# Kernel tuning notes

Hardware: AMD Instinct MI355X
Metric: run time of the kernel (lower is better)

## Reference

```python
import jax, jax.numpy as jnp
import numpy as np

NUM_HEADS = 16
EPS_LN = 1e-5
EPS_NORM = 1e-12


def layernorm(x, g, b):
    mu = jnp.mean(x, axis=-1, keepdims=True)
    var = jnp.mean((x - mu) ** 2, axis=-1, keepdims=True)
    return (x - mu) * jax.lax.rsqrt(var + EPS_LN) * g + b


def l2norm(x):
    n = jnp.sqrt(jnp.sum(x * x, axis=-1, keepdims=True))
    return x / jnp.maximum(n, EPS_NORM)


def setup_inputs() -> dict:
    key = jax.random.key(0)
    ks = jax.random.split(key, 12)
    B, N, C = 8, 1024, 1024
    std = 0.02
    inp = {
        "txt_token": jax.random.normal(ks[0], (B, 1, C), jnp.float32),
        "text_features": jax.random.normal(ks[1], (B, N, C), jnp.float32),
        "text_mask": jax.random.randint(ks[2], (B, N), 0, 2).astype(bool),
        "vis_token": jax.random.normal(ks[3], (B, 1, C), jnp.float32),
        "top_lens": 256,
        # parameters
        "Wqkv": jax.random.normal(ks[4], (C, 3 * C), jnp.float32) * std,
        "bqkv": jnp.zeros((3 * C,), jnp.float32),
        "Wp2": jax.random.normal(ks[5], (C, C), jnp.float32) * std,
        "bp2": jnp.zeros((C,), jnp.float32),
        "ln2_g": jnp.ones((C,), jnp.float32),
        "ln2_b": jnp.zeros((C,), jnp.float32),
        "sim_alpha": jnp.ones((1,), jnp.float32),
        "sim_beta": jnp.zeros((1,), jnp.float32),
        "Wp1": jax.random.normal(ks[6], (C, C), jnp.float32) * std,
        "bp1": jnp.zeros((C,), jnp.float32),
        "ln1_g": jnp.ones((C,), jnp.float32),
        "ln1_b": jnp.zeros((C,), jnp.float32),
    }
    return inp


def reference(txt_token, text_features, text_mask, vis_token, top_lens,
              Wqkv, bqkv, Wp2, bp2, ln2_g, ln2_b,
              sim_alpha, sim_beta, Wp1, bp1, ln1_g, ln1_b):
    B, N, C = text_features.shape
    H = NUM_HEADS
    hd = C // H
    scale = hd ** (-0.5)

    qkv = (text_features @ Wqkv + bqkv).reshape(B, N, 3, H, hd)
    q = qkv[:, :, 0].transpose(0, 2, 1, 3)  # [B,H,N,hd]
    k = qkv[:, :, 1].transpose(0, 2, 1, 3)
    v = qkv[:, :, 2].transpose(0, 2, 1, 3)

    attn = jnp.einsum('bhqd,bhkd->bhqk', q, k) * scale  # [B,H,N,N]
    vals, idx = jax.lax.top_k(attn, top_lens)            # [B,H,N,k]
    p = jax.nn.softmax(vals, axis=-1)

    # scatter topk softmax back into zeros at original key positions
    b_ix = jnp.arange(B)[:, None, None, None]
    h_ix = jnp.arange(H)[None, :, None, None]
    q_ix = jnp.arange(N)[None, None, :, None]
    attn_sp = jnp.zeros_like(attn).at[b_ix, h_ix, q_ix, idx].set(p)

    # mask padded keys, then second softmax (dropout = identity in eval)
    attn_sp = jnp.where(text_mask[:, None, None, :], -jnp.inf, attn_sp)
    attn_w = jax.nn.softmax(attn_sp, axis=-1)

    x = jnp.einsum('bhqk,bhkd->bqhd', attn_w, v).reshape(B, N, C)
    x = x @ Wp2 + bp2
    tf = layernorm(text_features + x, ln2_g, ln2_b)  # [B,N,C]

    # cosine-similarity top-k pooling
    sim = sim_beta + sim_alpha * jnp.einsum('bmc,bnc->bmn', l2norm(vis_token), l2norm(tf))  # [B,1,N]
    sim = jax.nn.sigmoid(jnp.where(text_mask[:, None, :], -jnp.inf, sim))
    _, top_idx = jax.lax.top_k(sim, top_lens)        # [B,1,k]
    top_idx = top_idx[:, 0]                           # [B,k]
    top_vecs = jnp.take_along_axis(tf, top_idx[:, :, None], axis=1)  # [B,k,C]
    pooled = jnp.mean(top_vecs, axis=1, keepdims=True)               # [B,1,C]

    tt = pooled + txt_token
    tt = layernorm(tt @ Wp1 + bp1, ln1_g, ln1_b)
    return tt, tf
```

## Files before the change

### kernel.cpp

```cpp
#include <hip/hip_runtime.h>
#include <stdint.h>

typedef unsigned short u16;
typedef float floatx4 __attribute__((ext_vector_type(4)));
typedef short short8 __attribute__((ext_vector_type(8)));

#define TOPK_ 256

#define AS1(p) ((const __attribute__((address_space(1))) void*)(p))
#define AS3(p) ((__attribute__((address_space(3))) void*)(p))

__device__ __forceinline__ u16 f2bf(float f) {
  unsigned u = __builtin_bit_cast(unsigned, f);
  unsigned r = (u + 0x7FFFu + ((u >> 16) & 1u)) >> 16;
  return (u16)r;
}
__device__ __forceinline__ float bf2f(u16 b) {
  unsigned u = ((unsigned)b) << 16;
  return __builtin_bit_cast(float, u);
}

__device__ __forceinline__ float wave_sum_f32(float x) {
#define DPP_STEP(ctrl, rmask)                                                        \
  {                                                                                  \
    float t_ = __builtin_bit_cast(                                                   \
        float, __builtin_amdgcn_update_dpp(0, __builtin_bit_cast(int, x), ctrl,      \
                                           rmask, 0xf, true));                       \
    x += t_;                                                                         \
  }
  DPP_STEP(0x111, 0xf)
  DPP_STEP(0x112, 0xf)
  DPP_STEP(0x114, 0xf)
  DPP_STEP(0x118, 0xf)
  DPP_STEP(0x142, 0xa)
  DPP_STEP(0x143, 0xc)
#undef DPP_STEP
  return __builtin_bit_cast(float,
                            __builtin_amdgcn_readlane(__builtin_bit_cast(int, x), 63));
}

__device__ __forceinline__ void wave_sum2_f32(float& x, float& y) {
#define DPP_STEP2(ctrl, rmask)                                                       \
  {                                                                                  \
    float tx_ = __builtin_bit_cast(                                                  \
        float, __builtin_amdgcn_update_dpp(0, __builtin_bit_cast(int, x), ctrl,      \
                                           rmask, 0xf, true));                       \
    float ty_ = __builtin_bit_cast(                                                  \
        float, __builtin_amdgcn_update_dpp(0, __builtin_bit_cast(int, y), ctrl,      \
                                           rmask, 0xf, true));                       \
    x += tx_;                                                                        \
    y += ty_;                                                                        \
  }
  DPP_STEP2(0x111, 0xf)
  DPP_STEP2(0x112, 0xf)
  DPP_STEP2(0x114, 0xf)
  DPP_STEP2(0x118, 0xf)
  DPP_STEP2(0x142, 0xa)
  DPP_STEP2(0x143, 0xc)
#undef DPP_STEP2
  x = __builtin_bit_cast(float, __builtin_amdgcn_readlane(__builtin_bit_cast(int, x), 63));
  y = __builtin_bit_cast(float, __builtin_amdgcn_readlane(__builtin_bit_cast(int, y), 63));
}

__device__ __forceinline__ float block_sum256(float v, volatile float* scratch, int wave,
                                              int lane) {
#pragma unroll
  for (int o = 32; o > 0; o >>= 1) v += __shfl_xor(v, o);
  __syncthreads();
  if (lane == 0) scratch[wave] = v;
  __syncthreads();
  return scratch[0] + scratch[1] + scratch[2] + scratch[3];
}

__global__ __launch_bounds__(256) void prep_kernel(const float* __restrict__ text,
                                                   u16* __restrict__ Abf,
                                                   const float* __restrict__ Wqkv,
                                                   u16* __restrict__ Wtqkv,
                                                   const float* __restrict__ Wp2,
                                                   u16* __restrict__ Wtp2,
                                                   const float* __restrict__ vis,
                                                   float* __restrict__ vhat) {
  __shared__ u16 tile[32][33];
  __shared__ float red[4];
  int blk = blockIdx.x, t = threadIdx.x;
  if (blk < 8192) {
    int i = (blk * 256 + t) * 4;
    float4 v = *reinterpret_cast<const float4*>(text + i);
    ushort4 o;
    o.x = f2bf(v.x); o.y = f2bf(v.y); o.z = f2bf(v.z); o.w = f2bf(v.w);
    *reinterpret_cast<ushort4*>(Abf + i) = o;
  } else if (blk < 12288) {
    const float* W;
    u16* Wt;
    int cols, id;
    if (blk < 11264) { W = Wqkv; Wt = Wtqkv; cols = 3072; id = blk - 8192; }
    else             { W = Wp2;  Wt = Wtp2;  cols = 1024; id = blk - 11264; }
    int nx = cols >> 5;
    int n0 = (id % nx) * 32, k0 = (id / nx) * 32;
    int r = t >> 3, c4 = (t & 7) * 4;
    float4 v = *reinterpret_cast<const float4*>(W + (size_t)(k0 + r) * cols + n0 + c4);
    tile[r][c4 + 0] = f2bf(v.x);
    tile[r][c4 + 1] = f2bf(v.y);
    tile[r][c4 + 2] = f2bf(v.z);
    tile[r][c4 + 3] = f2bf(v.w);
    __syncthreads();
    ushort4 o;
    o.x = tile[c4 + 0][r]; o.y = tile[c4 + 1][r];
    o.z = tile[c4 + 2][r]; o.w = tile[c4 + 3][r];
    *reinterpret_cast<ushort4*>(Wt + (size_t)(n0 + r) * 1024 + k0 + c4) = o;
  } else {
    int b = blk - 12288, wave = t >> 6, lane = t & 63;
    float4 vv = *reinterpret_cast<const float4*>(vis + b * 1024 + t * 4);
    float sq = vv.x * vv.x + vv.y * vv.y + vv.z * vv.z + vv.w * vv.w;
    sq = block_sum256(sq, red, wave, lane);
    float inv = 1.f / fmaxf(sqrtf(sq), 1e-12f);
    float4 o = make_float4(vv.x * inv, vv.y * inv, vv.z * inv, vv.w * inv);
    *reinterpret_cast<float4*>(vhat + b * 1024 + t * 4) = o;
  }
}

__global__ __launch_bounds__(256) void gemm_bt(const u16* __restrict__ A,
                                               const u16* __restrict__ Bt,
                                               const float* __restrict__ bias,
                                               int M, int Nn, int K, int mode,
                                               u16* __restrict__ qb, u16* __restrict__ kb,
                                               u16* __restrict__ vb, u16* __restrict__ yb) {
  __shared__ __align__(16) u16 SMEM[9216];
  u16* As = SMEM;
  u16* Bs = SMEM + 4096;
  int id = blockIdx.x + blockIdx.y * gridDim.x;
  int cpx = (gridDim.x * gridDim.y) >> 3;
  int swz = (id & 7) * cpx + (id >> 3);
  int bx = swz % gridDim.x, by = swz / gridDim.x;
  int m0 = by * 128, n0 = bx * 128;
  int t = threadIdx.x, lane = t & 63, wave = t >> 6;
  int wr = wave >> 1, wc = wave & 1;
  int lrow = lane & 15, lko = (lane >> 4) * 8;
  floatx4 acc[4][4];
#pragma unroll
  for (int i = 0; i < 4; ++i)
#pragma unroll
    for (int j = 0; j < 4; ++j) acc[i][j] = (floatx4){0.f, 0.f, 0.f, 0.f};
  int srow = t >> 2, sc8 = (t & 3) * 8;
  const u16* gA0 = A + (size_t)(m0 + srow) * K + sc8;
  const u16* gA1 = A + (size_t)(m0 + srow + 64) * K + sc8;
  const u16* gB0 = Bt + (size_t)(n0 + srow) * K + sc8;
  const u16* gB1 = Bt + (size_t)(n0 + srow + 64) * K + sc8;
  for (int k0 = 0; k0 < K; k0 += 32) {
    __syncthreads();
    __builtin_amdgcn_global_load_lds(AS1(gA0 + k0), AS3(&As[t * 8]), 16, 0, 0);
    __builtin_amdgcn_global_load_lds(AS1(gA1 + k0), AS3(&As[t * 8 + 2048]), 16, 0, 0);
    __builtin_amdgcn_global_load_lds(AS1(gB0 + k0), AS3(&Bs[t * 8]), 16, 0, 0);
    __builtin_amdgcn_global_load_lds(AS1(gB1 + k0), AS3(&Bs[t * 8 + 2048]), 16, 0, 0);
    __syncthreads();
    short8 afr[4], bfr[4];
#pragma unroll
    for (int i = 0; i < 4; ++i) {
      afr[i] = *reinterpret_cast<const short8*>(&As[(wr * 64 + i * 16 + lrow) * 32 + lko]);
      bfr[i] = *reinterpret_cast<const short8*>(&Bs[(wc * 64 + i * 16 + lrow) * 32 + lko]);
    }
#pragma unroll
    for (int i = 0; i < 4; ++i)
#pragma unroll
      for (int j = 0; j < 4; ++j)
        acc[i][j] = __builtin_amdgcn_mfma_f32_16x16x32_bf16(afr[i], bfr[j], acc[i][j], 0, 0, 0);
  }
  int rb = (lane >> 4) * 4;
  if (mode == 0 && n0 >= 2048) {
#pragma unroll
    for (int i = 0; i < 4; ++i) {
#pragma unroll
      for (int j = 0; j < 4; ++j) {
        int gcol = n0 + wc * 64 + j * 16 + lrow;
        float bv = bias[gcol];
        int grow0 = m0 + wr * 64 + i * 16 + rb;
        int cc = gcol & 1023, hh = cc >> 6, dd = cc & 63;
        int bb = grow0 >> 10, nq0 = grow0 & 1023;
        size_t headq = ((size_t)bb * 16 + hh);
        int dtile = dd >> 4, drow = dd & 15;
        int ks32 = nq0 >> 5, kk = nq0 & 31, lq = kk >> 3, e = kk & 7;
        int lane2 = lq * 16 + drow;
        ushort4 o;
        o.x = f2bf(acc[i][j][0] + bv);
        o.y = f2bf(acc[i][j][1] + bv);
        o.z = f2bf(acc[i][j][2] + bv);
        o.w = f2bf(acc[i][j][3] + bv);
        *reinterpret_cast<ushort4*>(vb + headq * 65536 + (size_t)ks32 * 2048 +
                                    dtile * 512 + lane2 * 8 + e) = o;
      }
    }
  } else {
    u16* LDSC = SMEM;
    for (int half = 0; half < 2; ++half) {
      __syncthreads();
      if (wc == half) {
#pragma unroll
        for (int i = 0; i < 4; ++i)
#pragma unroll
          for (int j = 0; j < 4; ++j) {
            float bv = bias[n0 + half * 64 + j * 16 + lrow];
#pragma unroll
            for (int rr = 0; rr < 4; ++rr)
              LDSC[(wr * 64 + i * 16 + rb + rr) * 72 + j * 16 + lrow] =
                  f2bf(acc[i][j][rr] + bv);
          }
      }
      __syncthreads();
      int row = t >> 4, c4 = (t & 15) * 4;
#pragma unroll
      for (int it = 0; it < 8; ++it) {
        int rw = row + it * 16;
        ushort4 val = *reinterpret_cast<const ushort4*>(&LDSC[rw * 72 + c4]);
        int grow = m0 + rw, gcol = n0 + half * 64 + c4;
        if (mode == 1) {
          *reinterpret_cast<ushort4*>(yb + (size_t)grow * 1024 + gcol) = val;
        } else {
          int sec = gcol >> 10, cc = gcol & 1023, hh = cc >> 6, dd = cc & 63;
          int bb = grow >> 10, nq = grow & 1023;
          size_t head = ((size_t)bb * 16 + hh);
          if (sec == 0) {
            *reinterpret_cast<ushort4*>(qb + (head * 1024 + nq) * 64 + dd) = val;
          } else {
            int kc = nq >> 4, krow = nq & 15;
            int p = dd >> 5, quad = (dd >> 3) & 3, e = dd & 7;
            *reinterpret_cast<ushort4*>(kb + head * 65536 + (size_t)kc * 1024 +
                                        p * 512 + (quad * 16 + krow) * 8 + e) = val;
          }
        }
      }
    }
  }
}

#define SSTR 1036
__global__ __launch_bounds__(512, 8) void attn_kernel(const u16* __restrict__ qb,
                                                      const u16* __restrict__ kb,
                                                      const u16* __restrict__ vb,
                                                      const int* __restrict__ mask,
                                                      u16* __restrict__ xout) {
  extern __shared__ __align__(16) char smem[];
  u16* Sb = reinterpret_cast<u16*>(smem);
  u16* qs = reinterpret_cast<u16*>(smem + 33152);
  unsigned char* mk8 = reinterpret_cast<unsigned char*>(smem + 35456);
  float* invZs = reinterpret_cast<float*>(smem + 36480);
  float* part = reinterpret_cast<float*>(smem + 36544);

  int blk = blockIdx.x;
  int bh = blk >> 6, qt = blk & 63;
  int b = bh >> 4, h = bh & 15;
  int t = threadIdx.x, wave = t >> 6, lane = t & 63;
  const u16* qh = qb + ((size_t)bh * 1024 + qt * 16) * 64;
  const u16* kh = kb + (size_t)bh * 65536;
  const u16* vh = vb + (size_t)bh * 65536;

  {
    int2 mm = *reinterpret_cast<const int2*>(mask + b * 1024 + t * 2);
    u16 pk = (u16)((mm.x != 0 ? 1u : 0u) | ((mm.y != 0 ? 1u : 0u) << 8));
    *reinterpret_cast<u16*>(&mk8[t * 2]) = pk;
  }
  if (t < 256) {
    int row = t >> 4, c4 = (t & 15) * 4;
    *reinterpret_cast<ushort4*>(&qs[row * 72 + c4]) =
        *reinterpret_cast<const ushort4*>(qh + row * 64 + c4);
  }
  __syncthreads();

  int lrow = lane & 15, lko = (lane >> 4) * 8;
  int quad = lane >> 4;
  int dtile = wave & 3, kq = wave >> 2;
  const u16* vbase = vh + (size_t)(kq * 16 * 4 + dtile) * 512 + lane * 8;

  {
    short8 qf0 = *reinterpret_cast<const short8*>(&qs[lrow * 72 + lko]);
    short8 qf1 = *reinterpret_cast<const short8*>(&qs[lrow * 72 + lko + 32]);
#pragma unroll 4
    for (int c = 0; c < 8; ++c) {
      int kc = wave * 8 + c;
      const u16* kt = kh + (size_t)kc * 1024 + lane * 8;
      short8 kf0 = *reinterpret_cast<const short8*>(kt);
      short8 kf1 = *reinterpret_cast<const short8*>(kt + 512);
      floatx4 acc = (floatx4){0.f, 0.f, 0.f, 0.f};
      acc = __builtin_amdgcn_mfma_f32_16x16x32_bf16(kf0, qf0, acc, 0, 0, 0);
      acc = __builtin_amdgcn_mfma_f32_16x16x32_bf16(kf1, qf1, acc, 0, 0, 0);
      unsigned kk[4];
#pragma unroll
      for (int i = 0; i < 4; ++i) {
        float f = __builtin_fmaf(acc[i], 64.f, 4096.f);
        f = __builtin_amdgcn_fmed3f(f, 0.f, 8191.f);
        kk[i] = (unsigned)f;
      }
      uint2 pk;
      pk.x = __builtin_amdgcn_perm(kk[1], kk[0], 0x05040100u);
      pk.y = __builtin_amdgcn_perm(kk[3], kk[2], 0x05040100u);
      *reinterpret_cast<uint2*>(&Sb[lrow * SSTR + kc * 16 + quad * 4]) = pk;
    }
  }
  __syncthreads();

  short8 vp0 = *reinterpret_cast<const short8*>(vbase);
  short8 vp1 = *reinterpret_cast<const short8*>(vbase + 2048);
  short8 vp2 = *reinterpret_cast<const short8*>(vbase + 4096);
  short8 vp3 = *reinterpret_cast<const short8*>(vbase + 6144);
  asm volatile("" : "+v"(vp0), "+v"(vp1), "+v"(vp2), "+v"(vp3));

  {
    const u16* SrA = Sb + (wave * 2) * SSTR;
    const u16* SrB = Sb + (wave * 2 + 1) * SSTR;
    unsigned kA[16], kB[16];
#pragma unroll
    for (int jj = 0; jj < 4; ++jj) {
      uint2 pa = *reinterpret_cast<const uint2*>(SrA + 4 * lane + 256 * jj);
      uint2 pb = *reinterpret_cast<const uint2*>(SrB + 4 * lane + 256 * jj);
      kA[4 * jj + 0] = pa.x & 0xffffu; kA[4 * jj + 1] = pa.x >> 16;
      kA[4 * jj + 2] = pa.y & 0xffffu; kA[4 * jj + 3] = pa.y >> 16;
      kB[4 * jj + 0] = pb.x & 0xffffu; kB[4 * jj + 1] = pb.x >> 16;
      kB[4 * jj + 2] = pb.y & 0xffffu; kB[4 * jj + 3] = pb.y >> 16;
    }
    unsigned TA = 0, TB = 0;
    int dA = 0, dB = 0;
    for (int bit = 12; bit >= 5; --bit) {
      unsigned cA = TA | (1u << bit), cB = TB | (1u << bit);
      int cntA = 0, cntB = 0;
#pragma unroll
      for (int i = 0; i < 16; ++i) {
        cntA += (int)__popcll(__ballot(kA[i] >= cA));
        cntB += (int)__popcll(__ballot(kB[i] >= cB));
      }
      if (!dA && cntA >= TOPK_) { TA = cA; if (cntA == TOPK_) dA = 1; }
      if (!dB && cntB >= TOPK_) { TB = cB; if (cntB == TOPK_) dB = 1; }
      if (dA && dB) break;
    }
    unsigned mm[4];
#pragma unroll
    for (int jj = 0; jj < 4; ++jj)
      mm[jj] = *reinterpret_cast<const unsigned*>(mk8 + 4 * lane + 256 * jj);
    const float C1 = 1.44269504f / 512.f;
    const float C0 = -4096.f * (1.44269504f / 512.f);
#pragma unroll 1
    for (int rr = 0; rr < 2; ++rr) {
      int row = wave * 2 + rr;
      unsigned T = rr ? TB : TA;
      unsigned kk[16];
      if (rr == 0) {
#pragma unroll
        for (int i = 0; i < 16; ++i) kk[i] = kA[i];
      } else {
        const u16* Sr = Sb + row * SSTR;
#pragma unroll
        for (int jj = 0; jj < 4; ++jj) {
          uint2 p = *reinterpret_cast<const uint2*>(Sr + 4 * lane + 256 * jj);
          kk[4 * jj + 0] = p.x & 0xffffu; kk[4 * jj + 1] = p.x >> 16;
          kk[4 * jj + 2] = p.y & 0xffffu; kk[4 * jj + 3] = p.y >> 16;
        }
      }
      float e[16];
      float seq[4] = {0.f, 0.f, 0.f, 0.f};
#pragma unroll
      for (int i = 0; i < 16; ++i) {
        float ex = __builtin_amdgcn_exp2f(__builtin_fmaf((float)kk[i], C1, C0));
        ex = (kk[i] >= T) ? ex : 0.f;
        e[i] = ex;
        seq[i & 3] += ex;
      }
      float se = wave_sum_f32((seq[0] + seq[1]) + (seq[2] + seq[3]));
      float cB2 = __builtin_amdgcn_rcpf(se) * 1.44269504f;
      float Z = 0.f;
      u16* Wr = Sb + row * SSTR;
#pragma unroll
      for (int jj = 0; jj < 4; ++jj) {
        unsigned m = mm[jj];
        float w0 = __builtin_amdgcn_exp2f(e[4 * jj + 0] * cB2);
        float w1 = __builtin_amdgcn_exp2f(e[4 * jj + 1] * cB2);
        float w2 = __builtin_amdgcn_exp2f(e[4 * jj + 2] * cB2);
        float w3 = __builtin_amdgcn_exp2f(e[4 * jj + 3] * cB2);
        w0 = (m & 0x000000ffu) ? 0.f : w0;
        w1 = (m & 0x0000ff00u) ? 0.f : w1;
        w2 = (m & 0x00ff0000u) ? 0.f : w2;
        w3 = (m & 0xff000000u) ? 0.f : w3;
        Z += (w0 + w1) + (w2 + w3);
        uint2 pw;
        pw.x = __builtin_amdgcn_perm(__builtin_bit_cast(unsigned, w1),
                                     __builtin_bit_cast(unsigned, w0), 0x07060302u);
        pw.y = __builtin_amdgcn_perm(__builtin_bit_cast(unsigned, w3),
                                     __builtin_bit_cast(unsigned, w2), 0x07060302u);
        *reinterpret_cast<uint2*>(Wr + 4 * lane + 256 * jj) = pw;
      }
      Z = wave_sum_f32(Z);
      if (lane == 0) invZs[row] = __builtin_amdgcn_rcpf(Z);
    }
  }
  __syncthreads();

  {
    floatx4 acc = (floatx4){0.f, 0.f, 0.f, 0.f};
    const u16* wrow = Sb + lrow * SSTR + kq * 512;
    short8 af;
    af = *reinterpret_cast<const short8*>(wrow + 0 * 32 + lko);
    acc = __builtin_amdgcn_mfma_f32_16x16x32_bf16(af, vp0, acc, 0, 0, 0);
    af = *reinterpret_cast<const short8*>(wrow + 1 * 32 + lko);
    acc = __builtin_amdgcn_mfma_f32_16x16x32_bf16(af, vp1, acc, 0, 0, 0);
    af = *reinterpret_cast<const short8*>(wrow + 2 * 32 + lko);
    acc = __builtin_amdgcn_mfma_f32_16x16x32_bf16(af, vp2, acc, 0, 0, 0);
    af = *reinterpret_cast<const short8*>(wrow + 3 * 32 + lko);
    acc = __builtin_amdgcn_mfma_f32_16x16x32_bf16(af, vp3, acc, 0, 0, 0);
#pragma unroll
    for (int ks = 4; ks < 16; ++ks) {
      short8 bf = *reinterpret_cast<const short8*>(vbase + (size_t)ks * 2048);
      short8 af2 = *reinterpret_cast<const short8*>(wrow + ks * 32 + lko);
      acc = __builtin_amdgcn_mfma_f32_16x16x32_bf16(af2, bf, acc, 0, 0, 0);
    }
    if (kq == 1)
      *reinterpret_cast<floatx4*>(part + (size_t)(dtile * 64 + lane) * 4) = acc;
    __syncthreads();
    if (kq == 0) {
      floatx4 p2 = *reinterpret_cast<const floatx4*>(part + (size_t)(dtile * 64 + lane) * 4);
      float4 iz = *reinterpret_cast<const float4*>(&invZs[quad * 4]);
      int d = dtile * 16 + lrow;
      u16* xo = xout + ((size_t)(b * 1024 + qt * 16 + quad * 4)) * 1024 + h * 64 + d;
      xo[0 * 1024] = f2bf((acc[0] + p2[0]) * iz.x);
      xo[1 * 1024] = f2bf((acc[1] + p2[1]) * iz.y);
      xo[2 * 1024] = f2bf((acc[2] + p2[2]) * iz.z);
      xo[3 * 1024] = f2bf((acc[3] + p2[3]) * iz.w);
    }
  }
}

__global__ void resid_ln(const u16* __restrict__ y,
                         const float* __restrict__ text,
                         const float* __restrict__ g,
                         const float* __restrict__ be,
                         const float* __restrict__ vhat,
                         const int* __restrict__ mask,
                         const float* __restrict__ alpha,
                         const float* __restrict__ beta,
                         float* __restrict__ tf,
                         float* __restrict__ sim_g) {
  int wave = threadIdx.x >> 6, lane = threadIdx.x & 63;
  int row = blockIdx.x * 8 + wave;
  int b = row >> 10;
  size_t rbase = (size_t)row * 1024;
  int c0 = lane * 4;
  float v[16];
  float s = 0.f, sq = 0.f;
#pragma unroll
  for (int i = 0; i < 4; ++i) {
    float4 tv = *reinterpret_cast<const float4*>(text + rbase + i * 256 + c0);
    ushort4 yv = *reinterpret_cast<const ushort4*>(y + rbase + i * 256 + c0);
    float a0 = bf2f(yv.x) + tv.x;
    float a1 = bf2f(yv.y) + tv.y;
    float a2 = bf2f(yv.z) + tv.z;
    float a3 = bf2f(yv.w) + tv.w;
    v[i * 4 + 0] = a0; v[i * 4 + 1] = a1; v[i * 4 + 2] = a2; v[i * 4 + 3] = a3;
    s += (a0 + a1) + (a2 + a3);
    sq += (a0 * a0 + a1 * a1) + (a2 * a2 + a3 * a3);
  }
  wave_sum2_f32(s, sq);
  float mean = s * (1.f / 1024.f);
  float var = sq * (1.f / 1024.f) - mean * mean;
  float rs = rsqrtf(var + 1e-5f);
  float s2 = 0.f, dd = 0.f;
#pragma unroll
  for (int i = 0; i < 4; ++i) {
    float4 gv = *reinterpret_cast<const float4*>(g + i * 256 + c0);
    float4 bv = *reinterpret_cast<const float4*>(be + i * 256 + c0);
    float4 hv = *reinterpret_cast<const float4*>(vhat + b * 1024 + i * 256 + c0);
    float o0 = (v[i * 4 + 0] - mean) * rs * gv.x + bv.x;
    float o1 = (v[i * 4 + 1] - mean) * rs * gv.y + bv.y;
    float o2 = (v[i * 4 + 2] - mean) * rs * gv.z + bv.z;
    float o3 = (v[i * 4 + 3] - mean) * rs * gv.w + bv.w;
    float4 ov = make_float4(o0, o1, o2, o3);
    *reinterpret_cast<float4*>(tf + rbase + i * 256 + c0) = ov;
    s2 += (o0 * o0 + o1 * o1) + (o2 * o2 + o3 * o3);
    dd += (o0 * hv.x + o1 * hv.y) + (o2 * hv.z + o3 * hv.w);
  }
  wave_sum2_f32(s2, dd);
  if (lane == 0) {
    float den = fmaxf(sqrtf(s2), 1e-12f);
    float sv = beta[0] + alpha[0] * dd / den;
    sim_g[row] = mask[row] ? -__builtin_inff() : sv;
  }
}

__global__ __launch_bounds__(256) void topk_pool(const float* __restrict__ sim_g,
                                                 const float* __restrict__ tf,
                                                 float* __restrict__ ttpre_acc) {
  __shared__ int idxl[256];
  __shared__ int scount;
  int b = blockIdx.x, p = blockIdx.y, t = threadIdx.x, lane = t & 63;
  if (t == 0) scount = 0;
  __syncthreads();
  if (t < 64) {
    unsigned uv[16];
#pragma unroll
    for (int j = 0; j < 16; ++j) {
      unsigned x = __builtin_bit_cast(unsigned, sim_g[b * 1024 + lane + 64 * j]);
      uv[j] = (x & 0x80000000u) ? ~x : (x | 0x80000000u);
    }
    unsigned T = 0;
    for (int bit = 31; bit >= 0; --bit) {
      unsigned cand = T | (1u << bit);
      int c = 0;
#pragma unroll
      for (int j = 0; j < 16; ++j) c += __popcll(__ballot(uv[j] >= cand));
      if (c >= TOPK_) {
        T = cand;
        if (c == TOPK_) break;
      }
    }
#pragma unroll
    for (int j = 0; j < 16; ++j) {
      if (uv[j] >= T) {
        int q = atomicAdd(&scount, 1);
        if (q < TOPK_) idxl[q] = lane + 64 * j;
      }
    }
  }
  __syncthreads();
  float4 pa = make_float4(0.f, 0.f, 0.f, 0.f);
  for (int i = p * 64; i < p * 64 + 64; ++i) {
    int n = idxl[i];
    float4 vr = *reinterpret_cast<const float4*>(tf + ((size_t)b * 1024 + n) * 1024 + t * 4);
    pa.x += vr.x; pa.y += vr.y; pa.z += vr.z; pa.w += vr.w;
  }
  atomicAdd(&ttpre_acc[b * 1024 + t * 4 + 0], pa.x);
  atomicAdd(&ttpre_acc[b * 1024 + t * 4 + 1], pa.y);
  atomicAdd(&ttpre_acc[b * 1024 + t * 4 + 2], pa.z);
  atomicAdd(&ttpre_acc[b * 1024 + t * 4 + 3], pa.w);
}

__global__ __launch_bounds__(256) void matvec_p1(const float* __restrict__ ttpre_acc,
                                                 const float* __restrict__ txt,
                                                 const float* __restrict__ Wp1,
                                                 const float* __restrict__ bp1,
                                                 float* __restrict__ ttv) {
  __shared__ float xs[1024];
  __shared__ float red[4][64];
  int b = blockIdx.x, q = blockIdx.y, t = threadIdx.x;
  for (int j = t; j < 1024; j += 256)
    xs[j] = ttpre_acc[b * 1024 + j] * (1.f / 256.f) + txt[b * 1024 + j];
  __syncthreads();
  int r = t >> 6, col = q * 64 + (t & 63);
  float acc = 0.f;
#pragma unroll 8
  for (int c = r * 256; c < r * 256 + 256; ++c) acc += xs[c] * Wp1[(size_t)c * 1024 + col];
  red[r][t & 63] = acc;
  __syncthreads();
  if (t < 64) {
    float o = red[0][t] + red[1][t] + red[2][t] + red[3][t] + bp1[q * 64 + t];
    ttv[b * 1024 + q * 64 + t] = o;
  }
}

__global__ __launch_bounds__(256) void ln_tt(const float* __restrict__ ttv,
                                             const float* __restrict__ g1,
                                             const float* __restrict__ b1,
                                             float* __restrict__ tt_out) {
  __shared__ float red[4];
  int b = blockIdx.x, t = threadIdx.x, wave = t >> 6, lane = t & 63;
  float4 v = *reinterpret_cast<const float4*>(ttv + b * 1024 + t * 4);
  float s = v.x + v.y + v.z + v.w;
  float sq = v.x * v.x + v.y * v.y + v.z * v.z + v.w * v.w;
  s = block_sum256(s, red, wave, lane);
  sq = block_sum256(sq, red, wave, lane);
  float mean = s * (1.f / 1024.f);
  float var = sq * (1.f / 1024.f) - mean * mean;
  float rs = rsqrtf(var + 1e-5f);
  float4 gv = *reinterpret_cast<const float4*>(g1 + t * 4);
  float4 bv = *reinterpret_cast<const float4*>(b1 + t * 4);
  float4 o;
  o.x = (v.x - mean) * rs * gv.x + bv.x;
  o.y = (v.y - mean) * rs * gv.y + bv.y;
  o.z = (v.z - mean) * rs * gv.z + bv.z;
  o.w = (v.w - mean) * rs * gv.w + bv.w;
  *reinterpret_cast<float4*>(tt_out + b * 1024 + t * 4) = o;
}

extern "C" void kernel_launch(void* const* d_in, const int* in_sizes, int n_in, void* d_out,
                              int out_size, void* d_ws, size_t ws_size, hipStream_t stream) {
  (void)in_sizes; (void)n_in; (void)out_size; (void)ws_size;
  const float* txt = (const float*)d_in[0];
  const float* text = (const float*)d_in[1];
  const int* mask = (const int*)d_in[2];
  const float* vis = (const float*)d_in[3];
  const float* Wqkv = (const float*)d_in[5];
  const float* bqkv = (const float*)d_in[6];
  const float* Wp2 = (const float*)d_in[7];
  const float* bp2 = (const float*)d_in[8];
  const float* g2 = (const float*)d_in[9];
  const float* b2 = (const float*)d_in[10];
  const float* alpha = (const float*)d_in[11];
  const float* beta = (const float*)d_in[12];
  const float* Wp1 = (const float*)d_in[13];
  const float* bp1 = (const float*)d_in[14];
  const float* g1 = (const float*)d_in[15];
  const float* b1 = (const float*)d_in[16];

  char* ws = (char*)d_ws;
  const size_t MB = 1u << 20;
  u16* Abf = (u16*)(ws);
  u16* Wtqkv = (u16*)(ws + 16 * MB);
  u16* Wtp2 = (u16*)(ws + 22 * MB);
  u16* qbuf = (u16*)(ws + 24 * MB);
  u16* kbuf = (u16*)(ws + 40 * MB);
  u16* vbuf = (u16*)(ws + 56 * MB);
  u16* ybuf = (u16*)(ws + 72 * MB);
  float* vhat = (float*)(ws + 88 * MB);
  float* sim_g = (float*)(ws + 88 * MB + 65536);
  float* ttpre = (float*)(ws + 88 * MB + 131072);
  float* ttv = (float*)(ws + 88 * MB + 196608);

  float* out = (float*)d_out;
  float* tt_out = out;
  float* tf_out = out + 8 * 1024;

  hipMemsetAsync(ttpre, 0, 8 * 1024 * sizeof(float), stream);
  prep_kernel<<<dim3(12296), dim3(256), 0, stream>>>(text, Abf, Wqkv, Wtqkv, Wp2, Wtp2, vis,
                                                     vhat);
  gemm_bt<<<dim3(24, 64), dim3(256), 0, stream>>>(Abf, Wtqkv, bqkv, 8192, 3072, 1024, 0, qbuf,
                                                  kbuf, vbuf, (u16*)nullptr);
  attn_kernel<<<dim3(8192), dim3(512), 40640, stream>>>(qbuf, kbuf, vbuf, mask, Abf);
  gemm_bt<<<dim3(8, 64), dim3(256), 0, stream>>>(Abf, Wtp2, bp2, 8192, 1024, 1024, 1,
                                                 (u16*)nullptr, (u16*)nullptr, (u16*)nullptr,
                                                 ybuf);
  resid_ln<<<dim3(1024), dim3(512), 0, stream>>>(ybuf, text, g2, b2, vhat, mask, alpha, beta,
                                                 tf_out, sim_g);
  topk_pool<<<dim3(8, 4), dim3(256), 0, stream>>>(sim_g, tf_out, ttpre);
  matvec_p1<<<dim3(8, 16), dim3(256), 0, stream>>>(ttpre, txt, Wp1, bp1, ttv);
  ln_tt<<<dim3(8), dim3(256), 0, stream>>>(ttv, g1, b1, tt_out);
}
```

Measured before the change: 453.9 us.

## Triple-buffer GEMM LDS tiles with async global_load_lds prefetch two steps ahead

The bf16 GEMM main loop now uses three LDS buffers and issues the global-to-LDS loads for tile k+2 before computing tile k. Explicit vmcnt waits and barriers replace the two syncthreads per iteration, so memory latency can overlap the MFMA work. This raises LDS use per block to 48KB, which may lower occupancy. The loop count is hardcoded to 32 K-tiles, which assumes K equals 1024.

```diff
diff --git a/kernel.cpp b/kernel.cpp
--- a/kernel.cpp
+++ b/kernel.cpp
@@ -125,9 +125,7 @@
                                                int M, int Nn, int K, int mode,
                                                u16* __restrict__ qb, u16* __restrict__ kb,
                                                u16* __restrict__ vb, u16* __restrict__ yb) {
-  __shared__ __align__(16) u16 SMEM[9216];
-  u16* As = SMEM;
-  u16* Bs = SMEM + 4096;
+  __shared__ __align__(16) u16 SMEM[24576];
   int id = blockIdx.x + blockIdx.y * gridDim.x;
   int cpx = (gridDim.x * gridDim.y) >> 3;
   int swz = (id & 7) * cpx + (id >> 3);
@@ -146,25 +144,51 @@
   const u16* gA1 = A + (size_t)(m0 + srow + 64) * K + sc8;
   const u16* gB0 = Bt + (size_t)(n0 + srow) * K + sc8;
   const u16* gB1 = Bt + (size_t)(n0 + srow + 64) * K + sc8;
-  for (int k0 = 0; k0 < K; k0 += 32) {
-    __syncthreads();
-    __builtin_amdgcn_global_load_lds(AS1(gA0 + k0), AS3(&As[t * 8]), 16, 0, 0);
-    __builtin_amdgcn_global_load_lds(AS1(gA1 + k0), AS3(&As[t * 8 + 2048]), 16, 0, 0);
-    __builtin_amdgcn_global_load_lds(AS1(gB0 + k0), AS3(&Bs[t * 8]), 16, 0, 0);
-    __builtin_amdgcn_global_load_lds(AS1(gB1 + k0), AS3(&Bs[t * 8 + 2048]), 16, 0, 0);
-    __syncthreads();
+
+#define STAGE_KT(ktv, bufv)                                                              \
+  {                                                                                      \
+    int koff_ = (ktv) * 32;                                                              \
+    u16* dst_ = SMEM + (bufv) * 8192 + t * 8;                                            \
+    __builtin_amdgcn_global_load_lds(AS1(gA0 + koff_), AS3(dst_), 16, 0, 0);             \
+    __builtin_amdgcn_global_load_lds(AS1(gA1 + koff_), AS3(dst_ + 2048), 16, 0, 0);      \
+    __builtin_amdgcn_global_load_lds(AS1(gB0 + koff_), AS3(dst_ + 4096), 16, 0, 0);      \
+    __builtin_amdgcn_global_load_lds(AS1(gB1 + koff_), AS3(dst_ + 6144), 16, 0, 0);      \
+  }
+
+  STAGE_KT(0, 0)
+  STAGE_KT(1, 1)
+  int cb = 0;
+  const int NKT = 32;
+#pragma unroll 1
+  for (int kt = 0; kt < NKT; ++kt) {
+    int kn = kt + 2;
+    if (kn < NKT) {
+      int bn = cb + 2; if (bn >= 3) bn -= 3;
+      STAGE_KT(kn, bn)
+    }
+    if (kt < NKT - 2)       asm volatile("s_waitcnt vmcnt(8)" ::: "memory");
+    else if (kt == NKT - 2) asm volatile("s_waitcnt vmcnt(4)" ::: "memory");
+    else                    asm volatile("s_waitcnt vmcnt(0)" ::: "memory");
+    __builtin_amdgcn_s_barrier();
+    const u16* Asb = SMEM + cb * 8192;
+    const u16* Bsb = Asb + 4096;
     short8 afr[4], bfr[4];
 #pragma unroll
     for (int i = 0; i < 4; ++i) {
-      afr[i] = *reinterpret_cast<const short8*>(&As[(wr * 64 + i * 16 + lrow) * 32 + lko]);
-      bfr[i] = *reinterpret_cast<const short8*>(&Bs[(wc * 64 + i * 16 + lrow) * 32 + lko]);
+      afr[i] = *reinterpret_cast<const short8*>(&Asb[(wr * 64 + i * 16 + lrow) * 32 + lko]);
+      bfr[i] = *reinterpret_cast<const short8*>(&Bsb[(wc * 64 + i * 16 + lrow) * 32 + lko]);
     }
 #pragma unroll
     for (int i = 0; i < 4; ++i)
 #pragma unroll
       for (int j = 0; j < 4; ++j)
         acc[i][j] = __builtin_amdgcn_mfma_f32_16x16x32_bf16(afr[i], bfr[j], acc[i][j], 0, 0, 0);
-  }
+    asm volatile("s_waitcnt lgkmcnt(0)" ::: "memory");
+    __builtin_amdgcn_s_barrier();
+    cb = (cb == 2) ? 0 : cb + 1;
+  }
+#undef STAGE_KT
+
   int rb = (lane >> 4) * 4;
   if (mode == 0 && n0 >= 2048) {
 #pragma unroll
```

After: 437.5 us. 1.04x faster.
